# Kernel tuning notes

Hardware: AMD Instinct MI355X
Metric: run time of the kernel (lower is better)

The kernel has to match this reference:

```python
import jax, jax.numpy as jnp
import numpy as np

MANIFOLD_K = 1.0   # Lorentz curvature manifold.k
POWER_K = 2        # power_k
EPS_PHI = 1e-6
EPS_FP = 1e-8

N, IN_C, OUT_C, H = 32768, 128, 128, 8


def setup_inputs() -> dict:
    key = jax.random.key(0)
    ks = jax.random.split(key, 11)
    s = 1.0 / np.sqrt(IN_C)  # nn.Linear default init scale
    u = lambda k, shape: jax.random.uniform(k, shape, jnp.float32, -s, s)
    return {
        "query_input": jax.random.normal(ks[0], (N, IN_C), jnp.float32),
        "source_input": jax.random.normal(ks[1], (N, IN_C), jnp.float32),
        "Wq_w": u(ks[2], (H, OUT_C, IN_C)),
        "Wq_b": u(ks[3], (H, OUT_C)),
        "Wk_w": u(ks[4], (H, OUT_C, IN_C)),
        "Wk_b": u(ks[5], (H, OUT_C)),
        "Wv_w": u(ks[6], (H, OUT_C, IN_C)),
        "Wv_b": u(ks[7], (H, OUT_C)),
        "v_map_w": u(ks[8], (OUT_C, OUT_C)),  # v_map_mlp acts on v (out_channels feats)
        "v_map_b": u(ks[9], (OUT_C,)),
        "norm_scale": jnp.ones((), jnp.float32),
    }


def _fp(x, p):
    # norm(x) / (norm(x**p) + eps) * x**p, norms over last dim
    norm_x = jnp.linalg.norm(x, axis=-1, keepdims=True)
    xp = x ** p
    norm_xp = jnp.linalg.norm(xp, axis=-1, keepdims=True)
    return norm_x / (norm_xp + EPS_FP) * xp


def reference(query_input, source_input, Wq_w, Wq_b, Wk_w, Wk_b, Wv_w, Wv_b,
              v_map_w, v_map_b, norm_scale):
    # Per-head HypLinear space part; the concatenated time coordinate is
    # immediately stripped by hyp_*[..., 1:] in linear_focus_attention,
    # so only the linear (space) output participates in the math.
    qs = jnp.einsum('ni,hoi->nho', query_input, Wq_w) + Wq_b   # [N,H,D]
    ks_ = jnp.einsum('ni,hoi->nho', source_input, Wk_w) + Wk_b  # [N,H,D]
    v = jnp.einsum('ni,hoi->nho', source_input, Wv_w) + Wv_b    # [N,H,D]

    denom_scale = jnp.abs(norm_scale) + EPS_PHI
    phi_qs = _fp((jax.nn.relu(qs) + EPS_PHI) / denom_scale, POWER_K)
    phi_ks = _fp((jax.nn.relu(ks_) + EPS_PHI) / denom_scale, POWER_K)

    k_transpose_v = jnp.einsum('nhm,nhd->hmd', phi_ks, v)        # [H,D,D]
    numerator = jnp.einsum('nhm,hmd->nhd', phi_qs, k_transpose_v)
    denominator = jnp.einsum('nhd,hd->nh', phi_qs, phi_ks.sum(axis=0))[..., None]
    attn_output = numerator / (denominator + EPS_PHI)            # [N,H,D]

    vss = jnp.einsum('nhd,od->nho', v, v_map_w) + v_map_b        # v_map_mlp(v)
    attn_output = attn_output + vss

    out = attn_output.mean(axis=1)                               # heads mean [N,D]
    out_time = jnp.sqrt(jnp.sum(out ** 2, axis=-1, keepdims=True) + MANIFOLD_K)
    return jnp.concatenate([out_time, out], axis=-1)             # [N,D+1]
```

## Files before the change

### kernel.cpp

```cpp
#include <hip/hip_runtime.h>

#define NTOK   32768
#define CDIM   128
#define NH     8
#define QT     32

typedef __bf16 bf16;
typedef __bf16 bf16x4v __attribute__((ext_vector_type(4)));
typedef __bf16 bf16x8v __attribute__((ext_vector_type(8)));
typedef float  f32x4   __attribute__((ext_vector_type(4)));

__device__ __forceinline__ f32x4 mfma16(bf16x8v a, bf16x8v b, f32x4 c) {
  return __builtin_amdgcn_mfma_f32_16x16x32_bf16(a, b, c, 0, 0, 0);
}

__device__ __forceinline__ float xred16(float v) {
  v += __shfl_xor(v, 1);
  v += __shfl_xor(v, 2);
  v += __shfl_xor(v, 4);
  v += __shfl_xor(v, 8);
  return v;
}

template<int CTRL>
__device__ __forceinline__ float dpp_add(float x) {
  int y = __builtin_amdgcn_mov_dpp(__float_as_int(x), CTRL, 0xf, 0xf, true);
  return x + __int_as_float(y);
}
__device__ __forceinline__ float xred16d(float v) {
  v = dpp_add<0xB1>(v);
  v = dpp_add<0x4E>(v);
  v = dpp_add<0x141>(v);
  v = dpp_add<0x140>(v);
  return v;
}

__device__ __forceinline__ int sidx(int row, int col) {
  return row * 128 + (col ^ ((row & 7) << 3));
}

__device__ __forceinline__ int tidx(int h, int tile, int kk, int lane) {
  return (((h * 8 + tile) * 4 + kk) * 64 + lane) * 8;
}

__global__ void __launch_bounds__(256) k_prepA(
    const float* __restrict__ src,
    const float* __restrict__ Wq, const float* __restrict__ Wk,
    const float* __restrict__ Wv, const float* __restrict__ Wv_b,
    bf16* __restrict__ srcT,
    bf16* __restrict__ wqT, bf16* __restrict__ wkT, bf16* __restrict__ wvT,
    float* __restrict__ Wvs, float* __restrict__ Wvbs)
{
  const int bid = blockIdx.x;
  const int tid = threadIdx.x;
  if (bid < 2048) {
    const int rb = bid;
    const int row = tid >> 4, col0 = (tid & 15) * 8;
    const float* p = src + (rb * 16 + row) * CDIM + col0;
    f32x4 v0 = *(const f32x4*)p;
    f32x4 v1 = *(const f32x4*)(p + 4);
    bf16x8v o;
    o[0] = (bf16)v0[0]; o[1] = (bf16)v0[1]; o[2] = (bf16)v0[2]; o[3] = (bf16)v0[3];
    o[4] = (bf16)v1[0]; o[5] = (bf16)v1[1]; o[6] = (bf16)v1[2]; o[7] = (bf16)v1[3];
    const int kk = col0 >> 5, lg = (col0 >> 3) & 3;
    const int lane = row + 16 * lg;
    *(bf16x8v*)(srcT + ((rb * 4 + kk) * 64 + lane) * 8) = o;
  } else {
    const int b = bid - 2048;
    const int h = b >> 6;
    const int o = (b & 63) * 2 + (tid >> 7);
    const int i = tid & 127;
    const int s = (h * CDIM + o) * CDIM + i;
    const int ot = o >> 4, l15 = o & 15;
    const int kk = i >> 5, lg = (i >> 3) & 3, j = i & 7;
    const int dst = tidx(h, ot, kk, l15 + 16 * lg) + j;
    wqT[dst] = (bf16)Wq[s];
    wkT[dst] = (bf16)Wk[s];
    wvT[dst] = (bf16)Wv[s];
    if (h == 0) {
      float sm = 0.f;
#pragma unroll
      for (int hh = 0; hh < NH; ++hh) sm += Wv[(hh * CDIM + o) * CDIM + i];
      Wvs[o * CDIM + i] = sm;
      if (o == 0) {
        float sb = 0.f;
#pragma unroll
        for (int hh = 0; hh < NH; ++hh) sb += Wv_b[hh * CDIM + i];
        Wvbs[i] = sb;
      }
    }
  }
}

__global__ void __launch_bounds__(256, 2) k_ktv(
    const bf16* __restrict__ srcT,
    const bf16* __restrict__ wkT, const bf16* __restrict__ wvT,
    const float* __restrict__ Wk_b, const float* __restrict__ Wv_b,
    bf16* __restrict__ ktv_part, float* __restrict__ ksum_part,
    int nsub, int cpx )
{
  const int x = blockIdx.x & 7;
  const int g = blockIdx.x >> 3;
  const int c = x * cpx + (g >> 3);
  const int h = g & 7;

  const int tid = threadIdx.x;
  const int w = tid >> 6, l = tid & 63;
  const int l15 = l & 15, lg = l >> 4;
  const int os = w * 32, owt = os >> 4;

  __shared__ bf16 s_phiT[128][68];
  __shared__ bf16 s_vT[128][68];
  __shared__ float s_red2[8][64];
  __shared__ float s_scale[64];

  const f32x4 z4 = {0.f, 0.f, 0.f, 0.f};

  bf16x8v bWk[2][4], bWv[2][4];
  float bK[2], bV[2];
#pragma unroll
  for (int ot = 0; ot < 2; ++ot) {
#pragma unroll
    for (int kk = 0; kk < 4; ++kk) {
      bWk[ot][kk] = *(const bf16x8v*)(wkT + tidx(h, owt + ot, kk, l));
      bWv[ot][kk] = *(const bf16x8v*)(wvT + tidx(h, owt + ot, kk, l));
    }
    bK[ot] = Wk_b[h * CDIM + os + ot * 16 + l15];
    bV[ot] = Wv_b[h * CDIM + os + ot * 16 + l15];
  }

  const int wd = (w >> 1) * 64, wm = (w & 1) * 64;
  f32x4 acc[4][4];
#pragma unroll
  for (int dt = 0; dt < 4; ++dt)
#pragma unroll
    for (int mt = 0; mt < 4; ++mt) acc[dt][mt] = z4;
  float ksacc[2] = {0.f, 0.f};

#pragma unroll 1
  for (int s = 0; s < nsub; ++s) {
    const int rbase = (c * nsub + s) * 4;
    f32x4 accK[4][2], accV[4][2];
#pragma unroll
    for (int nt = 0; nt < 4; ++nt)
#pragma unroll
      for (int ot = 0; ot < 2; ++ot) { accK[nt][ot] = z4; accV[nt][ot] = z4; }
#pragma unroll
    for (int kk = 0; kk < 4; ++kk) {
      bf16x8v a[4];
#pragma unroll
      for (int nt = 0; nt < 4; ++nt)
        a[nt] = *(const bf16x8v*)(srcT + (((rbase + nt) * 4 + kk) * 64 + l) * 8);
#pragma unroll
      for (int nt = 0; nt < 4; ++nt)
#pragma unroll
        for (int ot = 0; ot < 2; ++ot) {
          accK[nt][ot] = mfma16(a[nt], bWk[ot][kk], accK[nt][ot]);
          accV[nt][ot] = mfma16(a[nt], bWv[ot][kk], accV[nt][ot]);
        }
    }
    bf16x4v vq[4][2];
#pragma unroll
    for (int nt = 0; nt < 4; ++nt)
#pragma unroll
      for (int ot = 0; ot < 2; ++ot)
#pragma unroll
        for (int r = 0; r < 4; ++r)
          vq[nt][ot][r] = (bf16)(accV[nt][ot][r] + bV[ot]);
#pragma unroll
    for (int nt = 0; nt < 4; ++nt)
#pragma unroll
      for (int r = 0; r < 4; ++r) {
        float a2 = 0.f, a4 = 0.f;
#pragma unroll
        for (int ot = 0; ot < 2; ++ot) {
          float xv = fmaxf(accK[nt][ot][r] + bK[ot], 0.f) + 1e-6f;
          float x2 = xv * xv;
          accK[nt][ot][r] = x2;
          a2 += x2;
          a4 += x2 * x2;
        }
        a2 = xred16d(a2);
        a4 = xred16d(a4);
        if (l15 == 0) {
          s_red2[w * 2 + 0][nt * 16 + lg * 4 + r] = a2;
          s_red2[w * 2 + 1][nt * 16 + lg * 4 + r] = a4;
        }
      }
    __syncthreads();
    {
      float S2 = s_red2[0][l] + s_red2[2][l] + s_red2[4][l] + s_red2[6][l];
      float S4 = s_red2[1][l] + s_red2[3][l] + s_red2[5][l] + s_red2[7][l];
      s_scale[l] = sqrtf(S2) / (sqrtf(S4) + 1e-8f);
    }
#pragma unroll
    for (int nt = 0; nt < 4; ++nt) {
      f32x4 sc = *(const f32x4*)&s_scale[nt * 16 + lg * 4];
#pragma unroll
      for (int ot = 0; ot < 2; ++ot) {
        bf16x4v ph;
#pragma unroll
        for (int r = 0; r < 4; ++r) {
          float p = accK[nt][ot][r] * sc[r];
          ksacc[ot] += p;
          ph[r] = (bf16)p;
        }
        const int colb = os + ot * 16 + l15;
        *(bf16x4v*)&s_phiT[colb][nt * 16 + lg * 4] = ph;
        *(bf16x4v*)&s_vT[colb][nt * 16 + lg * 4] = vq[nt][ot];
      }
    }
    __syncthreads();
#pragma unroll
    for (int kkn = 0; kkn < 2; ++kkn) {
      bf16x8v aV[4], bP[4];
#pragma unroll
      for (int dt = 0; dt < 4; ++dt)
        aV[dt] = *(const bf16x8v*)&s_vT[wd + dt * 16 + l15][kkn * 32 + lg * 8];
#pragma unroll
      for (int mt = 0; mt < 4; ++mt)
        bP[mt] = *(const bf16x8v*)&s_phiT[wm + mt * 16 + l15][kkn * 32 + lg * 8];
#pragma unroll
      for (int dt = 0; dt < 4; ++dt)
#pragma unroll
        for (int mt = 0; mt < 4; ++mt)
          acc[dt][mt] = mfma16(aV[dt], bP[mt], acc[dt][mt]);
    }
  }

#pragma unroll
  for (int ot = 0; ot < 2; ++ot) {
    ksacc[ot] += __shfl_xor(ksacc[ot], 16);
    ksacc[ot] += __shfl_xor(ksacc[ot], 32);
  }
  if (l < 16) {
#pragma unroll
    for (int ot = 0; ot < 2; ++ot)
      ksum_part[(c * NH + h) * CDIM + os + ot * 16 + l] = ksacc[ot];
  }
  bf16* kp = ktv_part + ((c * NH + h) * 4 + w) * 4096;
#pragma unroll
  for (int dt = 0; dt < 4; ++dt)
#pragma unroll
    for (int mt = 0; mt < 4; ++mt) {
      bf16x4v q;
#pragma unroll
      for (int r = 0; r < 4; ++r) q[r] = (bf16)acc[dt][mt][r];
      *(bf16x4v*)(kp + ((dt * 4 + mt) * 64 + l) * 4) = q;
    }
}

__global__ void __launch_bounds__(256) k_finishB(
    const bf16* __restrict__ ktv_part, const float* __restrict__ ksum_part,
    const float* __restrict__ vmw, const float* __restrict__ vmb,
    const float* __restrict__ Wvs, const float* __restrict__ Wvbs,
    bf16* __restrict__ ktvT, bf16* __restrict__ ksb,
    bf16* __restrict__ w2sT, float* __restrict__ b2s, int nchunk)
{
  const int b = blockIdx.x;
  if (b < 512) {
    const int t = b * 256 + threadIdx.x;
    const int h = t >> 14;
    const int rem = t & 16383;
    const int d = rem >> 7, m = rem & 127;
    const int wq = ((d >> 6) << 1) | (m >> 6);
    const int dd = d & 63, mm = m & 63;
    const int dt = dd >> 4, r = dd & 3, lgp = (dd >> 2) & 3;
    const int mt = mm >> 4, l15p = mm & 15;
    const int lane = lgp * 16 + l15p;
    const int off = (h * 4 + wq) * 4096 + ((dt * 4 + mt) * 64 + lane) * 4 + r;
    float a = 0.f;
    for (int c = 0; c < nchunk; ++c)
      a += (float)ktv_part[c * (NH * 4 * 4096) + off];
    const int dtile = d >> 4, dl15 = d & 15;
    const int kk = m >> 5, mlg = (m >> 3) & 3, j = m & 7;
    ktvT[tidx(h, dtile, kk, dl15 + 16 * mlg) + j] = (bf16)a;
  } else if (b < 576) {
    const int t = (b - 512) * 256 + threadIdx.x;
    const int h = t >> 11;
    const int rem = t & 2047;
    const int kk = rem >> 9, lane = (rem >> 3) & 63, j = rem & 7;
    const int l15 = lane & 15, lg = lane >> 4;
    float a = 0.f;
    if (l15 == 0) {
      const int m = 32 * kk + 8 * lg + j;
      for (int c = 0; c < nchunk; ++c) a += ksum_part[(c * NH + h) * CDIM + m];
    }
    ksb[t] = (bf16)a;
  } else {
    const int sub = threadIdx.x >> 7, i = threadIdx.x & 127;
    const int o = (b - 576) * 2 + sub;
    __shared__ float s_vm[2][128];
    __shared__ float s_rd[2][128];
    s_vm[sub][i] = vmw[o * CDIM + i];
    __syncthreads();
    float acc = 0.f;
    for (int d = 0; d < CDIM; ++d) acc = fmaf(s_vm[sub][d], Wvs[d * CDIM + i], acc);
    const int ot = o >> 4, l15 = o & 15;
    const int kk = i >> 5, lg = (i >> 3) & 3, j = i & 7;
    w2sT[tidx(0, ot, kk, l15 + 16 * lg) + j] = (bf16)acc;
    s_rd[sub][i] = s_vm[sub][i] * Wvbs[i];
    __syncthreads();
    for (int st = 64; st > 0; st >>= 1) {
      if (i < st) s_rd[sub][i] += s_rd[sub][i + st];
      __syncthreads();
    }
    if (i == 0) b2s[o] = s_rd[sub][0] + 8.f * vmb[o];
  }
}

__global__ void __launch_bounds__(256, 2) k_out(
    const float* __restrict__ query, const bf16* __restrict__ srcT,
    const bf16* __restrict__ wqT, const float* __restrict__ Wq_b,
    const bf16* __restrict__ ktvT, const bf16* __restrict__ ksb,
    const bf16* __restrict__ w2sT, const float* __restrict__ b2s,
    float* __restrict__ out)
{
  const int nb = blockIdx.x * QT;
  const int tid = threadIdx.x;
  const int w = tid >> 6, l = tid & 63;
  const int l15 = l & 15, lg = l >> 4;
  const int os = w * 32, owt = os >> 4;

  __shared__ bf16 s_q[QT * 128];
  __shared__ bf16 s_phi[2][QT * 128];
  __shared__ float s_time[4][QT] __attribute__((aligned(16)));

  const f32x4 z4 = {0.f, 0.f, 0.f, 0.f};

#pragma unroll
  for (int j = 0; j < 4; ++j) {
    const int flat = tid + j * 256;
    const int n = flat >> 5, c4 = (flat & 31) * 4;
    f32x4 vq = *(const f32x4*)(query + (nb + n) * CDIM + c4);
    bf16x4v bq;
    bq[0] = (bf16)vq[0]; bq[1] = (bf16)vq[1]; bq[2] = (bf16)vq[2]; bq[3] = (bf16)vq[3];
    *(bf16x4v*)&s_q[sidx(n, c4)] = bq;
  }

  f32x4 accO[2][2];
#pragma unroll
  for (int nt = 0; nt < 2; ++nt)
#pragma unroll
    for (int ot = 0; ot < 2; ++ot) accO[nt][ot] = z4;

  __syncthreads();

  bf16x8v aq[2][4];
#pragma unroll
  for (int nt = 0; nt < 2; ++nt)
#pragma unroll
    for (int kk = 0; kk < 4; ++kk)
      aq[nt][kk] = *(const bf16x8v*)&s_q[sidx(nt * 16 + l15, kk * 32 + lg * 8)];

  for (int h = 0; h < NH; ++h) {
    bf16x8v wf[2][4], kf[2][4], kt[4];
#pragma unroll
    for (int ot = 0; ot < 2; ++ot)
#pragma unroll
      for (int kk = 0; kk < 4; ++kk) {
        wf[ot][kk] = *(const bf16x8v*)(wqT + tidx(h, owt + ot, kk, l));
        kf[ot][kk] = *(const bf16x8v*)(ktvT + tidx(h, owt + ot, kk, l));
      }
#pragma unroll
    for (int kk = 0; kk < 4; ++kk)
      kt[kk] = *(const bf16x8v*)(ksb + ((h * 4 + kk) * 64 + l) * 8);
    float bQ[2];
#pragma unroll
    for (int ot = 0; ot < 2; ++ot) bQ[ot] = Wq_b[h * CDIM + os + ot * 16 + l15];

    f32x4 accQ[2][2];
#pragma unroll
    for (int nt = 0; nt < 2; ++nt)
#pragma unroll
      for (int ot = 0; ot < 2; ++ot) accQ[nt][ot] = z4;
#pragma unroll
    for (int kk = 0; kk < 4; ++kk)
#pragma unroll
      for (int ot = 0; ot < 2; ++ot)
#pragma unroll
        for (int nt = 0; nt < 2; ++nt)
          accQ[nt][ot] = mfma16(aq[nt][kk], wf[ot][kk], accQ[nt][ot]);

    bf16* ph = s_phi[h & 1];
#pragma unroll
    for (int nt = 0; nt < 2; ++nt)
#pragma unroll
      for (int ot = 0; ot < 2; ++ot)
#pragma unroll
        for (int r = 0; r < 4; ++r) {
          float x = fmaxf(accQ[nt][ot][r] + bQ[ot], 0.f) + 1e-6f;
          ph[sidx(nt * 16 + lg * 4 + r, os + ot * 16 + l15)] = (bf16)(x * x);
        }
    __syncthreads();

    bf16x8v ap[2][4];
#pragma unroll
    for (int nt = 0; nt < 2; ++nt)
#pragma unroll
      for (int kk = 0; kk < 4; ++kk)
        ap[nt][kk] = *(const bf16x8v*)&ph[sidx(nt * 16 + l15, kk * 32 + lg * 8)];

    f32x4 accN[2][2], accT[2];
#pragma unroll
    for (int nt = 0; nt < 2; ++nt) {
      accT[nt] = z4;
#pragma unroll
      for (int dt = 0; dt < 2; ++dt) accN[nt][dt] = z4;
    }
#pragma unroll
    for (int kk = 0; kk < 4; ++kk) {
#pragma unroll
      for (int dt = 0; dt < 2; ++dt)
#pragma unroll
        for (int nt = 0; nt < 2; ++nt)
          accN[nt][dt] = mfma16(ap[nt][kk], kf[dt][kk], accN[nt][dt]);
#pragma unroll
      for (int nt = 0; nt < 2; ++nt)
        accT[nt] = mfma16(ap[nt][kk], kt[kk], accT[nt]);
    }
#pragma unroll
    for (int nt = 0; nt < 2; ++nt)
#pragma unroll
      for (int r = 0; r < 4; ++r) {
        float tr = __shfl(accT[nt][r], l & 48);
        float m = 1.0f / tr;
#pragma unroll
        for (int dt = 0; dt < 2; ++dt)
          accO[nt][dt][r] = fmaf(accN[nt][dt][r], m, accO[nt][dt][r]);
      }
  }

  const int rb0 = blockIdx.x * 2;
#pragma unroll
  for (int kk = 0; kk < 4; ++kk) {
    bf16x8v a[2];
#pragma unroll
    for (int nt = 0; nt < 2; ++nt)
      a[nt] = *(const bf16x8v*)(srcT + (((rb0 + nt) * 4 + kk) * 64 + l) * 8);
#pragma unroll
    for (int ot = 0; ot < 2; ++ot) {
      bf16x8v bw = *(const bf16x8v*)(w2sT + tidx(0, owt + ot, kk, l));
#pragma unroll
      for (int nt = 0; nt < 2; ++nt)
        accO[nt][ot] = mfma16(a[nt], bw, accO[nt][ot]);
    }
  }
  float bb[2];
#pragma unroll
  for (int ot = 0; ot < 2; ++ot) bb[ot] = b2s[os + ot * 16 + l15];

  float ps[2][4];
#pragma unroll
  for (int nt = 0; nt < 2; ++nt)
#pragma unroll
    for (int r = 0; r < 4; ++r) ps[nt][r] = 0.f;
#pragma unroll
  for (int nt = 0; nt < 2; ++nt)
#pragma unroll
    for (int ot = 0; ot < 2; ++ot)
#pragma unroll
      for (int r = 0; r < 4; ++r) {
        float v = (accO[nt][ot][r] + bb[ot]) * 0.125f;
        accO[nt][ot][r] = v;
        ps[nt][r] += v * v;
      }
#pragma unroll
  for (int nt = 0; nt < 2; ++nt)
#pragma unroll
    for (int r = 0; r < 4; ++r) {
      float t = xred16d(ps[nt][r]);
      if (l15 == 0) s_time[w][nt * 16 + lg * 4 + r] = t;
    }
#pragma unroll
  for (int nt = 0; nt < 2; ++nt)
#pragma unroll
    for (int ot = 0; ot < 2; ++ot)
#pragma unroll
      for (int r = 0; r < 4; ++r)
        out[(nb + nt * 16 + lg * 4 + r) * 129 + 1 + os + ot * 16 + l15] = accO[nt][ot][r];
  __syncthreads();
  if (tid < QT) {
    float S = 1.0f + s_time[0][tid] + s_time[1][tid] + s_time[2][tid] + s_time[3][tid];
    out[(nb + tid) * 129] = sqrtf(S);
  }
}

extern "C" void kernel_launch(void* const* d_in, const int* in_sizes, int n_in,
                              void* d_out, int out_size, void* d_ws, size_t ws_size,
                              hipStream_t stream) {
  const float* query  = (const float*)d_in[0];
  const float* source = (const float*)d_in[1];
  const float* Wq_w   = (const float*)d_in[2];
  const float* Wq_b   = (const float*)d_in[3];
  const float* Wk_w   = (const float*)d_in[4];
  const float* Wk_b   = (const float*)d_in[5];
  const float* Wv_w   = (const float*)d_in[6];
  const float* Wv_b   = (const float*)d_in[7];
  const float* vmw    = (const float*)d_in[8];
  const float* vmb    = (const float*)d_in[9];

  char* ws = (char*)d_ws;
  bf16*  wqT       = (bf16*)(ws + 0);
  bf16*  wkT       = (bf16*)(ws + 262144);
  bf16*  wvT       = (bf16*)(ws + 524288);
  bf16*  w2sT      = (bf16*)(ws + 786432);
  float* b2s       = (float*)(ws + 819200);
  float* Wvs       = (float*)(ws + 819712);
  float* Wvbs      = (float*)(ws + 885248);
  bf16*  ktvT      = (bf16*)(ws + 885760);
  bf16*  ksb       = (bf16*)(ws + 1147904);
  bf16*  srcT      = (bf16*)(ws + 1180672);
  float* ksum_part = (float*)(ws + 9569280);
  bf16*  ktv_part  = (bf16*)(ws + 10093568);

  int nchunk = 64, nsub = 8;
  if (ws_size < 10093568ull + 64ull * 262144ull) { nchunk = 32; nsub = 16; }

  k_prepA<<<2560, 256, 0, stream>>>(source, Wq_w, Wk_w, Wv_w, Wv_b,
                                    srcT, wqT, wkT, wvT, Wvs, Wvbs);
  k_ktv<<<nchunk * NH, 256, 0, stream>>>(srcT, wkT, wvT, Wk_b, Wv_b,
                                         ktv_part, ksum_part, nsub, nchunk / 8);
  k_finishB<<<640, 256, 0, stream>>>(ktv_part, ksum_part, vmw, vmb, Wvs, Wvbs,
                                     ktvT, ksb, w2sT, b2s, nchunk);
  k_out<<<NTOK / QT, 256, 0, stream>>>(query, srcT, wqT, Wq_b, ktvT, ksb,
                                       w2sT, b2s, (float*)d_out);
}
```

Baseline: 121.0 us.

## Process two heads per iteration in k_out to halve barriers

The per-head loop in the output kernel now handles head pairs. Both heads' Q projections are computed together, both phi tiles are written to a double-buffered shared array, and a single barrier is shared by the pair. The second head's ktv and ksum fragments are loaded after the barrier to limit register pressure. This halves the number of __syncthreads and exposes more independent MFMA work, at the cost of extra shared memory (16KB more) and more live registers, which may reduce occupancy.

Result: faster. 117.2 us (-3.1%).

```diff
diff --git a/kernel.cpp b/kernel.cpp
--- a/kernel.cpp
+++ b/kernel.cpp
@@ -12,14 +12,6 @@
 
 __device__ __forceinline__ f32x4 mfma16(bf16x8v a, bf16x8v b, f32x4 c) {
   return __builtin_amdgcn_mfma_f32_16x16x32_bf16(a, b, c, 0, 0, 0);
-}
-
-__device__ __forceinline__ float xred16(float v) {
-  v += __shfl_xor(v, 1);
-  v += __shfl_xor(v, 2);
-  v += __shfl_xor(v, 4);
-  v += __shfl_xor(v, 8);
-  return v;
 }
 
 template<int CTRL>
@@ -97,7 +89,7 @@
     const bf16* __restrict__ wkT, const bf16* __restrict__ wvT,
     const float* __restrict__ Wk_b, const float* __restrict__ Wv_b,
     bf16* __restrict__ ktv_part, float* __restrict__ ksum_part,
-    int nsub, int cpx )
+    int nsub, int cpx)
 {
   const int x = blockIdx.x & 7;
   const int g = blockIdx.x >> 3;
@@ -323,7 +315,7 @@
   const int os = w * 32, owt = os >> 4;
 
   __shared__ bf16 s_q[QT * 128];
-  __shared__ bf16 s_phi[2][QT * 128];
+  __shared__ bf16 s_phi[2][2][QT * 128];
   __shared__ float s_time[4][QT] __attribute__((aligned(16)));
 
   const f32x4 z4 = {0.f, 0.f, 0.f, 0.f};
@@ -353,82 +345,142 @@
     for (int kk = 0; kk < 4; ++kk)
       aq[nt][kk] = *(const bf16x8v*)&s_q[sidx(nt * 16 + l15, kk * 32 + lg * 8)];
 
-  for (int h = 0; h < NH; ++h) {
-    bf16x8v wf[2][4], kf[2][4], kt[4];
+#pragma unroll 1
+  for (int hp = 0; hp < 4; ++hp) {
+    const int h0 = hp * 2, h1 = h0 + 1;
+    const int pb = hp & 1;
+    bf16x8v wf0[2][4], wf1[2][4], kf0[2][4], kt0[4];
 #pragma unroll
     for (int ot = 0; ot < 2; ++ot)
 #pragma unroll
       for (int kk = 0; kk < 4; ++kk) {
-        wf[ot][kk] = *(const bf16x8v*)(wqT + tidx(h, owt + ot, kk, l));
-        kf[ot][kk] = *(const bf16x8v*)(ktvT + tidx(h, owt + ot, kk, l));
+        wf0[ot][kk] = *(const bf16x8v*)(wqT + tidx(h0, owt + ot, kk, l));
+        wf1[ot][kk] = *(const bf16x8v*)(wqT + tidx(h1, owt + ot, kk, l));
+        kf0[ot][kk] = *(const bf16x8v*)(ktvT + tidx(h0, owt + ot, kk, l));
       }
 #pragma unroll
     for (int kk = 0; kk < 4; ++kk)
-      kt[kk] = *(const bf16x8v*)(ksb + ((h * 4 + kk) * 64 + l) * 8);
-    float bQ[2];
-#pragma unroll
-    for (int ot = 0; ot < 2; ++ot) bQ[ot] = Wq_b[h * CDIM + os + ot * 16 + l15];
-
-    f32x4 accQ[2][2];
+      kt0[kk] = *(const bf16x8v*)(ksb + ((h0 * 4 + kk) * 64 + l) * 8);
+    float bQ0[2], bQ1[2];
+#pragma unroll
+    for (int ot = 0; ot < 2; ++ot) {
+      bQ0[ot] = Wq_b[h0 * CDIM + os + ot * 16 + l15];
+      bQ1[ot] = Wq_b[h1 * CDIM + os + ot * 16 + l15];
+    }
+
+    f32x4 accQ0[2][2], accQ1[2][2];
 #pragma unroll
     for (int nt = 0; nt < 2; ++nt)
 #pragma unroll
-      for (int ot = 0; ot < 2; ++ot) accQ[nt][ot] = z4;
+      for (int ot = 0; ot < 2; ++ot) { accQ0[nt][ot] = z4; accQ1[nt][ot] = z4; }
 #pragma unroll
     for (int kk = 0; kk < 4; ++kk)
 #pragma unroll
       for (int ot = 0; ot < 2; ++ot)
 #pragma unroll
+        for (int nt = 0; nt < 2; ++nt) {
+          accQ0[nt][ot] = mfma16(aq[nt][kk], wf0[ot][kk], accQ0[nt][ot]);
+          accQ1[nt][ot] = mfma16(aq[nt][kk], wf1[ot][kk], accQ1[nt][ot]);
+        }
+
+    bf16* ph0 = s_phi[pb][0];
+    bf16* ph1 = s_phi[pb][1];
+#pragma unroll
+    for (int nt = 0; nt < 2; ++nt)
+#pragma unroll
+      for (int ot = 0; ot < 2; ++ot)
+#pragma unroll
+        for (int r = 0; r < 4; ++r) {
+          const int ro = sidx(nt * 16 + lg * 4 + r, os + ot * 16 + l15);
+          float x0 = fmaxf(accQ0[nt][ot][r] + bQ0[ot], 0.f) + 1e-6f;
+          float x1 = fmaxf(accQ1[nt][ot][r] + bQ1[ot], 0.f) + 1e-6f;
+          ph0[ro] = (bf16)(x0 * x0);
+          ph1[ro] = (bf16)(x1 * x1);
+        }
+    __syncthreads();
+
+    bf16x8v kf1[2][4], kt1[4];
+#pragma unroll
+    for (int ot = 0; ot < 2; ++ot)
+#pragma unroll
+      for (int kk = 0; kk < 4; ++kk)
+        kf1[ot][kk] = *(const bf16x8v*)(ktvT + tidx(h1, owt + ot, kk, l));
+#pragma unroll
+    for (int kk = 0; kk < 4; ++kk)
+      kt1[kk] = *(const bf16x8v*)(ksb + ((h1 * 4 + kk) * 64 + l) * 8);
+
+    {
+      bf16x8v ap[2][4];
+#pragma unroll
+      for (int nt = 0; nt < 2; ++nt)
+#pragma unroll
+        for (int kk = 0; kk < 4; ++kk)
+          ap[nt][kk] = *(const bf16x8v*)&ph0[sidx(nt * 16 + l15, kk * 32 + lg * 8)];
+      f32x4 accN[2][2], accT[2];
+#pragma unroll
+      for (int nt = 0; nt < 2; ++nt) {
+        accT[nt] = z4;
+#pragma unroll
+        for (int dt = 0; dt < 2; ++dt) accN[nt][dt] = z4;
+      }
+#pragma unroll
+      for (int kk = 0; kk < 4; ++kk) {
+#pragma unroll
+        for (int dt = 0; dt < 2; ++dt)
+#pragma unroll
+          for (int nt = 0; nt < 2; ++nt)
+            accN[nt][dt] = mfma16(ap[nt][kk], kf0[dt][kk], accN[nt][dt]);
+#pragma unroll
         for (int nt = 0; nt < 2; ++nt)
-          accQ[nt][ot] = mfma16(aq[nt][kk], wf[ot][kk], accQ[nt][ot]);
-
-    bf16* ph = s_phi[h & 1];
-#pragma unroll
-    for (int nt = 0; nt < 2; ++nt)
-#pragma unroll
-      for (int ot = 0; ot < 2; ++ot)
+          accT[nt] = mfma16(ap[nt][kk], kt0[kk], accT[nt]);
+      }
+#pragma unroll
+      for (int nt = 0; nt < 2; ++nt)
 #pragma unroll
         for (int r = 0; r < 4; ++r) {
-          float x = fmaxf(accQ[nt][ot][r] + bQ[ot], 0.f) + 1e-6f;
-          ph[sidx(nt * 16 + lg * 4 + r, os + ot * 16 + l15)] = (bf16)(x * x);
-        }
-    __syncthreads();
-
-    bf16x8v ap[2][4];
-#pragma unroll
-    for (int nt = 0; nt < 2; ++nt)
-#pragma unroll
-      for (int kk = 0; kk < 4; ++kk)
-        ap[nt][kk] = *(const bf16x8v*)&ph[sidx(nt * 16 + l15, kk * 32 + lg * 8)];
-
-    f32x4 accN[2][2], accT[2];
-#pragma unroll
-    for (int nt = 0; nt < 2; ++nt) {
-      accT[nt] = z4;
-#pragma unroll
-      for (int dt = 0; dt < 2; ++dt) accN[nt][dt] = z4;
-    }
-#pragma unroll
-    for (int kk = 0; kk < 4; ++kk) {
-#pragma unroll
-      for (int dt = 0; dt < 2; ++dt)
+          float tr = __shfl(accT[nt][r], l & 48);
+          float m = 1.0f / tr;
+#pragma unroll
+          for (int dt = 0; dt < 2; ++dt)
+            accO[nt][dt][r] = fmaf(accN[nt][dt][r], m, accO[nt][dt][r]);
+        }
+    }
+    {
+      bf16x8v ap[2][4];
+#pragma unroll
+      for (int nt = 0; nt < 2; ++nt)
+#pragma unroll
+        for (int kk = 0; kk < 4; ++kk)
+          ap[nt][kk] = *(const bf16x8v*)&ph1[sidx(nt * 16 + l15, kk * 32 + lg * 8)];
+      f32x4 accN[2][2], accT[2];
+#pragma unroll
+      for (int nt = 0; nt < 2; ++nt) {
+        accT[nt] = z4;
+#pragma unroll
+        for (int dt = 0; dt < 2; ++dt) accN[nt][dt] = z4;
+      }
+#pragma unroll
+      for (int kk = 0; kk < 4; ++kk) {
+#pragma unroll
+        for (int dt = 0; dt < 2; ++dt)
+#pragma unroll
+          for (int nt = 0; nt < 2; ++nt)
+            accN[nt][dt] = mfma16(ap[nt][kk], kf1[dt][kk], accN[nt][dt]);
 #pragma unroll
         for (int nt = 0; nt < 2; ++nt)
-          accN[nt][dt] = mfma16(ap[nt][kk], kf[dt][kk], accN[nt][dt]);
+          accT[nt] = mfma16(ap[nt][kk], kt1[kk], accT[nt]);
+      }
 #pragma unroll
       for (int nt = 0; nt < 2; ++nt)
-        accT[nt] = mfma16(ap[nt][kk], kt[kk], accT[nt]);
-    }
-#pragma unroll
-    for (int nt = 0; nt < 2; ++nt)
-#pragma unroll
-      for (int r = 0; r < 4; ++r) {
-        float tr = __shfl(accT[nt][r], l & 48);
-        float m = 1.0f / tr;
-#pragma unroll
-        for (int dt = 0; dt < 2; ++dt)
-          accO[nt][dt][r] = fmaf(accN[nt][dt][r], m, accO[nt][dt][r]);
-      }
+#pragma unroll
+        for (int r = 0; r < 4; ++r) {
+          float tr = __shfl(accT[nt][r], l & 48);
+          float m = 1.0f / tr;
+#pragma unroll
+          for (int dt = 0; dt < 2; ++dt)
+            accO[nt][dt][r] = fmaf(accN[nt][dt][r], m, accO[nt][dt][r]);
+        }
+    }
   }
 
   const int rb0 = blockIdx.x * 2;
```

## Split k_out head loop into phi-compute and attention phases with one barrier

Applied to the files above, without the earlier changes.

The per-head loop in k_out is split in two. The first loop computes phi_q for all eight heads into a per-head shared buffer (s_phi grows from 2 to NH slots). A single __syncthreads then precedes a second loop that does the numerator and denominator MFMAs. This removes the per-head barriers but raises shared memory per block from about 16KB to 64KB for s_phi, which may cut occupancy below the two blocks per CU the launch bounds target. It also drops an unused shuffle reduction helper.

Measured after the change: 122.9 us. Within noise of the previous version (+1.5%).

```diff
diff --git a/kernel.cpp b/kernel.cpp
--- a/kernel.cpp
+++ b/kernel.cpp
@@ -12,14 +12,6 @@
 
 __device__ __forceinline__ f32x4 mfma16(bf16x8v a, bf16x8v b, f32x4 c) {
   return __builtin_amdgcn_mfma_f32_16x16x32_bf16(a, b, c, 0, 0, 0);
-}
-
-__device__ __forceinline__ float xred16(float v) {
-  v += __shfl_xor(v, 1);
-  v += __shfl_xor(v, 2);
-  v += __shfl_xor(v, 4);
-  v += __shfl_xor(v, 8);
-  return v;
 }
 
 template<int CTRL>
@@ -97,7 +89,7 @@
     const bf16* __restrict__ wkT, const bf16* __restrict__ wvT,
     const float* __restrict__ Wk_b, const float* __restrict__ Wv_b,
     bf16* __restrict__ ktv_part, float* __restrict__ ksum_part,
-    int nsub, int cpx )
+    int nsub, int cpx)
 {
   const int x = blockIdx.x & 7;
   const int g = blockIdx.x >> 3;
@@ -323,7 +315,7 @@
   const int os = w * 32, owt = os >> 4;
 
   __shared__ bf16 s_q[QT * 128];
-  __shared__ bf16 s_phi[2][QT * 128];
+  __shared__ bf16 s_phi[NH][QT * 128];
   __shared__ float s_time[4][QT] __attribute__((aligned(16)));
 
   const f32x4 z4 = {0.f, 0.f, 0.f, 0.f};
@@ -353,47 +345,57 @@
     for (int kk = 0; kk < 4; ++kk)
       aq[nt][kk] = *(const bf16x8v*)&s_q[sidx(nt * 16 + l15, kk * 32 + lg * 8)];
 
+#pragma unroll 1
   for (int h = 0; h < NH; ++h) {
-    bf16x8v wf[2][4], kf[2][4], kt[4];
+    bf16x8v wf[2][4];
 #pragma unroll
     for (int ot = 0; ot < 2; ++ot)
 #pragma unroll
-      for (int kk = 0; kk < 4; ++kk) {
+      for (int kk = 0; kk < 4; ++kk)
         wf[ot][kk] = *(const bf16x8v*)(wqT + tidx(h, owt + ot, kk, l));
+    float bQ[2];
+#pragma unroll
+    for (int ot = 0; ot < 2; ++ot) bQ[ot] = Wq_b[h * CDIM + os + ot * 16 + l15];
+
+    f32x4 accQ[2][2];
+#pragma unroll
+    for (int nt = 0; nt < 2; ++nt)
+#pragma unroll
+      for (int ot = 0; ot < 2; ++ot) accQ[nt][ot] = z4;
+#pragma unroll
+    for (int kk = 0; kk < 4; ++kk)
+#pragma unroll
+      for (int ot = 0; ot < 2; ++ot)
+#pragma unroll
+        for (int nt = 0; nt < 2; ++nt)
+          accQ[nt][ot] = mfma16(aq[nt][kk], wf[ot][kk], accQ[nt][ot]);
+
+    bf16* ph = s_phi[h];
+#pragma unroll
+    for (int nt = 0; nt < 2; ++nt)
+#pragma unroll
+      for (int ot = 0; ot < 2; ++ot)
+#pragma unroll
+        for (int r = 0; r < 4; ++r) {
+          float xv = fmaxf(accQ[nt][ot][r] + bQ[ot], 0.f) + 1e-6f;
+          ph[sidx(nt * 16 + lg * 4 + r, os + ot * 16 + l15)] = (bf16)(xv * xv);
+        }
+  }
+  __syncthreads();
+
+#pragma unroll 1
+  for (int h = 0; h < NH; ++h) {
+    bf16x8v kf[2][4], kt[4];
+#pragma unroll
+    for (int ot = 0; ot < 2; ++ot)
+#pragma unroll
+      for (int kk = 0; kk < 4; ++kk)
         kf[ot][kk] = *(const bf16x8v*)(ktvT + tidx(h, owt + ot, kk, l));
-      }
 #pragma unroll
     for (int kk = 0; kk < 4; ++kk)
       kt[kk] = *(const bf16x8v*)(ksb + ((h * 4 + kk) * 64 + l) * 8);
-    float bQ[2];
-#pragma unroll
-    for (int ot = 0; ot < 2; ++ot) bQ[ot] = Wq_b[h * CDIM + os + ot * 16 + l15];
-
-    f32x4 accQ[2][2];
-#pragma unroll
-    for (int nt = 0; nt < 2; ++nt)
-#pragma unroll
-      for (int ot = 0; ot < 2; ++ot) accQ[nt][ot] = z4;
-#pragma unroll
-    for (int kk = 0; kk < 4; ++kk)
-#pragma unroll
-      for (int ot = 0; ot < 2; ++ot)
-#pragma unroll
-        for (int nt = 0; nt < 2; ++nt)
-          accQ[nt][ot] = mfma16(aq[nt][kk], wf[ot][kk], accQ[nt][ot]);
-
-    bf16* ph = s_phi[h & 1];
-#pragma unroll
-    for (int nt = 0; nt < 2; ++nt)
-#pragma unroll
-      for (int ot = 0; ot < 2; ++ot)
-#pragma unroll
-        for (int r = 0; r < 4; ++r) {
-          float x = fmaxf(accQ[nt][ot][r] + bQ[ot], 0.f) + 1e-6f;
-          ph[sidx(nt * 16 + lg * 4 + r, os + ot * 16 + l15)] = (bf16)(x * x);
-        }
-    __syncthreads();
-
+
+    const bf16* ph = s_phi[h];
     bf16x8v ap[2][4];
 #pragma unroll
     for (int nt = 0; nt < 2; ++nt)
```
